# Performance work log

Measured on AMD Instinct MI355X. Metric: run time of the kernel, lower is better.

Reference implementation:

```python
import jax, jax.numpy as jnp
import numpy as np

NEG = -1e9


def setup_inputs() -> dict:
    key = jax.random.key(0)
    kq, kk, kv, ke = jax.random.split(key, 4)
    B, H, S, D = 4, 16, 2048, 64
    q = jax.random.normal(kq, (B, H, S, D), dtype=jnp.float32)
    k = jax.random.normal(kk, (B, H, S, D), dtype=jnp.float32)
    v = jax.random.normal(kv, (B, H, S, D), dtype=jnp.float32)
    event_length = jax.random.randint(ke, (B,), 0, S, dtype=jnp.int32)
    return {"q": q, "k": k, "v": v, "event_length": event_length}


def reference(q, k, v, event_length):
    B, H, S, D = q.shape
    scale = jnp.sqrt(jnp.asarray(D, dtype=jnp.float32))
    # [b,h,s,q] scores
    scores = jnp.einsum('bhsd,bhqd->bhsq', q, k) / scale
    idx = jnp.arange(S)
    el = event_length[:, None]  # [B,1]
    valid = idx[None, :] < el   # [B,S]
    # mask[b,s,q] = valid[b,s] & valid[b,q]; broadcast over heads
    mask = (valid[:, None, :, None] & valid[:, None, None, :])  # [B,1,S,S]
    scores = jnp.where(mask, scores, NEG)
    attn = jax.nn.softmax(scores, axis=-1)
    # dropout p=0.0 (eval): identity
    out = jnp.einsum('bhsq,bhqd->bhsd', attn, v)
    return out
```

## Files before the change

kernel.cpp:

```cpp
#include <hip/hip_runtime.h>
#include <hip/hip_bf16.h>


#define SQ 2048
#define DH 64
#define NBH 64
#define TK 64
#define LDE 72

typedef __attribute__((ext_vector_type(4))) float f32x4;
typedef __attribute__((ext_vector_type(8))) short bf16x8;
typedef __attribute__((ext_vector_type(4))) unsigned int u32x4;
typedef __attribute__((ext_vector_type(2))) unsigned int u32x2;

__device__ __forceinline__ unsigned int pk2(float lo, float hi) {
    __hip_bfloat162 h = __float22bfloat162_rn(float2{lo, hi});
    union { __hip_bfloat162 h; unsigned int u; } c; c.h = h;
    return c.u;
}

__global__ __launch_bounds__(256)
void meanv_k(const float* __restrict__ V, float* __restrict__ MV) {
    const int bh  = blockIdx.x >> 4;
    const int seg = blockIdx.x & 15;
    const float* vp = V + ((size_t)bh * SQ + (size_t)seg * 128) * DH;
    const int c = threadIdx.x & 15;
    const int r = threadIdx.x >> 4;
    const float* p = vp + (size_t)r * DH + c * 4;
    f32x4 s0 = *(const f32x4*)(p);
    f32x4 s1 = *(const f32x4*)(p + 16 * DH);
    f32x4 s2 = *(const f32x4*)(p + 32 * DH);
    f32x4 s3 = *(const f32x4*)(p + 48 * DH);
    s0 += *(const f32x4*)(p + 64 * DH);
    s1 += *(const f32x4*)(p + 80 * DH);
    s2 += *(const f32x4*)(p + 96 * DH);
    s3 += *(const f32x4*)(p + 112 * DH);
    f32x4 s = (s0 + s1) + (s2 + s3);
    __shared__ f32x4 red[16][16];
    red[r][c] = s;
    __syncthreads();
    if (threadIdx.x < 16) {
        f32x4 a = red[0][threadIdx.x];
        #pragma unroll
        for (int j = 1; j < 16; ++j) a += red[j][threadIdx.x];
        const float inv = 1.0f / (float)SQ;
        atomicAdd(&MV[bh * DH + threadIdx.x * 4 + 0], a[0] * inv);
        atomicAdd(&MV[bh * DH + threadIdx.x * 4 + 1], a[1] * inv);
        atomicAdd(&MV[bh * DH + threadIdx.x * 4 + 2], a[2] * inv);
        atomicAdd(&MV[bh * DH + threadIdx.x * 4 + 3], a[3] * inv);
    }
}

__global__ __launch_bounds__(256, 3)
void flash5(const float* __restrict__ Q, const float* __restrict__ K,
            const float* __restrict__ V, const int* __restrict__ EL,
            const float* __restrict__ MV, float* __restrict__ O,
            int* __restrict__ ticket) {
    const int t = threadIdx.x;

    {
        const int bh0    = blockIdx.x & (NBH - 1);
        const int qbase0 = (blockIdx.x >> 6) * 128;
        const int el0    = EL[bh0 >> 4];
        if (qbase0 >= el0) {
            float* Op = O + (size_t)bh0 * SQ * DH;
            const int c16 = t & 15, r0 = t >> 4;
            f32x4 mv = *(const f32x4*)(MV + bh0 * DH + c16 * 4);
            #pragma unroll
            for (int i = 0; i < 8; ++i)
                *(f32x4*)(Op + (size_t)(qbase0 + r0 + i * 16) * DH + c16 * 4) = mv;
        }
    }

    const int el0 = EL[0], el1 = EL[1], el2 = EL[2], el3 = EL[3];
    const int v0 = (el0 + 127) >> 7, v1 = (el1 + 127) >> 7;
    const int v2 = (el2 + 127) >> 7, v3 = (el3 + 127) >> 7;
    const int n0 = 16 * v0, n1 = n0 + 16 * v1, n2 = n1 + 16 * v2;
    const int nvalid = n2 + 16 * v3;

    __shared__ short Kb[TK][LDE];
    __shared__ short Vt[DH][LDE];
    __shared__ short Pl[4][32][LDE];
    __shared__ int item_s;

    const int wq = t >> 6, lane = t & 63, qd = lane >> 4, c = lane & 15;

    const int ksrow = t >> 2;
    const int ksdc  = t & 3;
    const int vpair = t & 31;
    const int vdg   = t >> 5;

    for (;;) {
        if (t == 0) item_s = atomicAdd(ticket, 1);
        __syncthreads();
        const int it = item_s;
        if (it >= nvalid) break;

        int b, u, vb, el;
        if      (it < n0) { b = 0; u = it;      vb = v0; el = el0; }
        else if (it < n1) { b = 1; u = it - n0; vb = v1; el = el1; }
        else if (it < n2) { b = 2; u = it - n1; vb = v2; el = el2; }
        else              { b = 3; u = it - n2; vb = v3; el = el3; }
        const int head  = u / vb;
        const int qt    = u - head * vb;
        const int bh    = b * 16 + head;
        const int qbase = qt * 128;

        const size_t base = (size_t)bh * SQ * DH;
        const float* Qp = Q + base;
        const float* Kp = K + base;
        const float* Vp = V + base;
        float* Op = O + base;

        const float sc = 0.125f * 1.44269504f;
        bf16x8 qf[2][2];
        #pragma unroll
        for (int nt = 0; nt < 2; ++nt) {
            const int row = qbase + wq * 32 + nt * 16 + c;
            #pragma unroll
            for (int kc = 0; kc < 2; ++kc) {
                const float* p = Qp + (size_t)row * DH + kc * 32 + qd * 8;
                f32x4 a  = *(const f32x4*)p;
                f32x4 bb = *(const f32x4*)(p + 4);
                u32x4 f;
                f[0] = pk2(a[0] * sc, a[1] * sc);
                f[1] = pk2(a[2] * sc, a[3] * sc);
                f[2] = pk2(bb[0] * sc, bb[1] * sc);
                f[3] = pk2(bb[2] * sc, bb[3] * sc);
                qf[nt][kc] = *(bf16x8*)&f;
            }
        }

        float l_[2] = {0.f, 0.f};
        f32x4 oacc[4][2];
        #pragma unroll
        for (int dt = 0; dt < 4; ++dt)
            #pragma unroll
            for (int nt = 0; nt < 2; ++nt)
                oacc[dt][nt] = (f32x4){0.f, 0.f, 0.f, 0.f};

        const int nkt = (el + TK - 1) / TK;

        f32x4 kg0, kg1, kg2, kg3, vg0, vg1, vg2, vg3;
        {
            const float* kp = Kp + (size_t)ksrow * DH + ksdc * 16;
            kg0 = *(const f32x4*)kp;
            kg1 = *(const f32x4*)(kp + 4);
            kg2 = *(const f32x4*)(kp + 8);
            kg3 = *(const f32x4*)(kp + 12);
            const float* vp0 = Vp + (size_t)(2 * vpair) * DH + vdg * 8;
            vg0 = *(const f32x4*)vp0;
            vg1 = *(const f32x4*)(vp0 + 4);
            vg2 = *(const f32x4*)(vp0 + DH);
            vg3 = *(const f32x4*)(vp0 + DH + 4);
        }

        for (int kt = 0; kt < nkt; ++kt) {
            const int k0 = kt * TK;

            __syncthreads();
            {
                u32x4 w0, w1;
                w0[0] = pk2(kg0[0], kg0[1]); w0[1] = pk2(kg0[2], kg0[3]);
                w0[2] = pk2(kg1[0], kg1[1]); w0[3] = pk2(kg1[2], kg1[3]);
                w1[0] = pk2(kg2[0], kg2[1]); w1[1] = pk2(kg2[2], kg2[3]);
                w1[2] = pk2(kg3[0], kg3[1]); w1[3] = pk2(kg3[2], kg3[3]);
                *(u32x4*)&Kb[ksrow][ksdc * 16]     = w0;
                *(u32x4*)&Kb[ksrow][ksdc * 16 + 8] = w1;
            }
            {
                #pragma unroll
                for (int i = 0; i < 4; ++i) {
                    *(unsigned int*)&Vt[vdg * 8 + i][2 * vpair]     = pk2(vg0[i], vg2[i]);
                    *(unsigned int*)&Vt[vdg * 8 + 4 + i][2 * vpair] = pk2(vg1[i], vg3[i]);
                }
            }
            __syncthreads();

            if (kt + 1 < nkt) {
                const int kn = k0 + TK;
                const float* kp = Kp + (size_t)(kn + ksrow) * DH + ksdc * 16;
                kg0 = *(const f32x4*)kp;
                kg1 = *(const f32x4*)(kp + 4);
                kg2 = *(const f32x4*)(kp + 8);
                kg3 = *(const f32x4*)(kp + 12);
                const float* vp0 = Vp + (size_t)(kn + 2 * vpair) * DH + vdg * 8;
                vg0 = *(const f32x4*)vp0;
                vg1 = *(const f32x4*)(vp0 + 4);
                vg2 = *(const f32x4*)(vp0 + DH);
                vg3 = *(const f32x4*)(vp0 + DH + 4);
            }

            f32x4 st[4][2];
            #pragma unroll
            for (int mt = 0; mt < 4; ++mt) {
                bf16x8 a0 = *(const bf16x8*)&Kb[mt * 16 + c][qd * 8];
                bf16x8 a1 = *(const bf16x8*)&Kb[mt * 16 + c][32 + qd * 8];
                #pragma unroll
                for (int nt = 0; nt < 2; ++nt) {
                    f32x4 acc = (f32x4){0.f, 0.f, 0.f, 0.f};
                    acc = __builtin_amdgcn_mfma_f32_16x16x32_bf16(a0, qf[nt][0], acc, 0, 0, 0);
                    acc = __builtin_amdgcn_mfma_f32_16x16x32_bf16(a1, qf[nt][1], acc, 0, 0, 0);
                    st[mt][nt] = acc;
                }
            }

            if (k0 + TK > el) {
                #pragma unroll
                for (int mt = 0; mt < 4; ++mt)
                    #pragma unroll
                    for (int r = 0; r < 4; ++r)
                        if (k0 + mt * 16 + qd * 4 + r >= el) {
                            st[mt][0][r] = -1e30f;
                            st[mt][1][r] = -1e30f;
                        }
            }

            #pragma unroll
            for (int nt = 0; nt < 2; ++nt) {
                #pragma unroll
                for (int mt = 0; mt < 4; ++mt) {
                    const float p0 = exp2f(st[mt][nt][0]);
                    const float p1 = exp2f(st[mt][nt][1]);
                    const float p2 = exp2f(st[mt][nt][2]);
                    const float p3 = exp2f(st[mt][nt][3]);
                    l_[nt] += (p0 + p1) + (p2 + p3);
                    u32x2 pw;
                    pw[0] = pk2(p0, p1);
                    pw[1] = pk2(p2, p3);
                    *(u32x2*)&Pl[wq][nt * 16 + c][mt * 16 + qd * 4] = pw;
                }
            }

            #pragma unroll
            for (int kc = 0; kc < 2; ++kc) {
                bf16x8 pb0 = *(const bf16x8*)&Pl[wq][c][kc * 32 + qd * 8];
                bf16x8 pb1 = *(const bf16x8*)&Pl[wq][16 + c][kc * 32 + qd * 8];
                #pragma unroll
                for (int dt = 0; dt < 4; ++dt) {
                    bf16x8 vf = *(const bf16x8*)&Vt[dt * 16 + c][kc * 32 + qd * 8];
                    oacc[dt][0] = __builtin_amdgcn_mfma_f32_16x16x32_bf16(vf, pb0, oacc[dt][0], 0, 0, 0);
                    oacc[dt][1] = __builtin_amdgcn_mfma_f32_16x16x32_bf16(vf, pb1, oacc[dt][1], 0, 0, 0);
                }
            }
        }

        #pragma unroll
        for (int nt = 0; nt < 2; ++nt) {
            l_[nt] += __shfl_xor(l_[nt], 16);
            l_[nt] += __shfl_xor(l_[nt], 32);
        }

        #pragma unroll
        for (int nt = 0; nt < 2; ++nt) {
            const int row = qbase + wq * 32 + nt * 16 + c;
            if (row < el) {
                const float inv = 1.0f / l_[nt];
                #pragma unroll
                for (int dt = 0; dt < 4; ++dt) {
                    f32x4 o = oacc[dt][nt];
                    o[0] *= inv; o[1] *= inv; o[2] *= inv; o[3] *= inv;
                    *(f32x4*)(Op + (size_t)row * DH + dt * 16 + qd * 4) = o;
                }
            } else {
                #pragma unroll
                for (int dt = 0; dt < 4; ++dt) {
                    f32x4 mv = *(const f32x4*)(MV + bh * DH + dt * 16 + qd * 4);
                    *(f32x4*)(Op + (size_t)row * DH + dt * 16 + qd * 4) = mv;
                }
            }
        }
    }
}

extern "C" void kernel_launch(void* const* d_in, const int* in_sizes, int n_in,
                              void* d_out, int out_size, void* d_ws, size_t ws_size,
                              hipStream_t stream) {
    const float* q  = (const float*)d_in[0];
    const float* k  = (const float*)d_in[1];
    const float* v  = (const float*)d_in[2];
    const int*   el = (const int*)d_in[3];
    float* out = (float*)d_out;
    float* mv  = (float*)d_ws;
    int*   tk  = (int*)((char*)d_ws + NBH * DH * sizeof(float));

    hipMemsetAsync(d_ws, 0, NBH * DH * sizeof(float) + 64, stream);
    meanv_k<<<dim3(NBH * 16), dim3(256), 0, stream>>>(v, mv);
    flash5<<<dim3(NBH * (SQ / 128)), dim3(256), 0, stream>>>(q, k, v, el, mv, out, tk);
}
```

Measured before the change: 203.3 us.

## Pre-convert K/V to swizzled bf16 tiles and stream them with async LDS loads

Adds a prepass kernel that converts K and V to bf16 in a pre-swizzled, pre-transposed tile layout and fuses the mean-of-V computation into it. The main attention kernel then uses 512-thread blocks with 8 waves and double-buffered direct global-to-LDS async copies, so the fp32 conversion and transpose no longer run inside the inner loop. This spends an extra workspace pass and 16 MB of scratch in exchange for halving the K/V bytes read per tile and overlapping loads with MFMA. The old path is kept as a fallback when the workspace is too small.

```diff
diff --git a/kernel.cpp b/kernel.cpp
--- a/kernel.cpp
+++ b/kernel.cpp
@@ -6,7 +6,10 @@
 #define DH 64
 #define NBH 64
 #define TK 64
+#define NTILE 32
+#define TILE_B 8192
 #define LDE 72
+#define LVP 68
 
 typedef __attribute__((ext_vector_type(4))) float f32x4;
 typedef __attribute__((ext_vector_type(8))) short bf16x8;
@@ -18,6 +21,257 @@
     union { __hip_bfloat162 h; unsigned int u; } c; c.h = h;
     return c.u;
 }
+
+__device__ __forceinline__ float bfu16_to_f(unsigned short s) {
+    union { unsigned int u; float f; } c; c.u = ((unsigned int)s) << 16;
+    return c.f;
+}
+
+__device__ __forceinline__ void async_cp16(const void* g, void* l) {
+    __builtin_amdgcn_global_load_lds(
+        (const __attribute__((address_space(1))) unsigned int*)g,
+        (__attribute__((address_space(3))) unsigned int*)l, 16, 0, 0);
+}
+
+
+__global__ __launch_bounds__(256)
+void convkv(const float* __restrict__ K, const float* __restrict__ V,
+            const int* __restrict__ EL, float* __restrict__ MV,
+            char* __restrict__ Kbt, char* __restrict__ Vbt) {
+    const int bh = blockIdx.x >> 5;
+    const int kt = blockIdx.x & 31;
+    const int k0 = kt * TK;
+    const int el = EL[bh >> 4];
+    const int t = threadIdx.x;
+    const int r  = t >> 2;
+    const int dc = t & 3;
+
+    __shared__ short LV[64][LVP];
+
+    {
+        const float* vp = V + ((size_t)bh * SQ + k0 + r) * DH + dc * 16;
+        f32x4 a = *(const f32x4*)vp;
+        f32x4 b = *(const f32x4*)(vp + 4);
+        f32x4 c2 = *(const f32x4*)(vp + 8);
+        f32x4 d2 = *(const f32x4*)(vp + 12);
+        u32x4 w0, w1;
+        w0[0] = pk2(a[0], a[1]);  w0[1] = pk2(a[2], a[3]);
+        w0[2] = pk2(b[0], b[1]);  w0[3] = pk2(b[2], b[3]);
+        w1[0] = pk2(c2[0], c2[1]); w1[1] = pk2(c2[2], c2[3]);
+        w1[2] = pk2(d2[0], d2[1]); w1[3] = pk2(d2[2], d2[3]);
+        *(u32x4*)&LV[r][dc * 16]     = w0;
+        *(u32x4*)&LV[r][dc * 16 + 8] = w1;
+    }
+
+    if (k0 < el) {
+        const float* kp = K + ((size_t)bh * SQ + k0 + r) * DH + dc * 16;
+        f32x4 a = *(const f32x4*)kp;
+        f32x4 b = *(const f32x4*)(kp + 4);
+        f32x4 c2 = *(const f32x4*)(kp + 8);
+        f32x4 d2 = *(const f32x4*)(kp + 12);
+        u32x4 w0, w1;
+        w0[0] = pk2(a[0], a[1]);  w0[1] = pk2(a[2], a[3]);
+        w0[2] = pk2(b[0], b[1]);  w0[3] = pk2(b[2], b[3]);
+        w1[0] = pk2(c2[0], c2[1]); w1[1] = pk2(c2[2], c2[3]);
+        w1[2] = pk2(d2[0], d2[1]); w1[3] = pk2(d2[2], d2[3]);
+        char* kb = Kbt + (size_t)(bh * NTILE + kt) * TILE_B + r * 128;
+        *(u32x4*)(kb + (((dc * 2)     ^ (r & 7)) << 4)) = w0;
+        *(u32x4*)(kb + (((dc * 2 + 1) ^ (r & 7)) << 4)) = w1;
+    }
+
+    __syncthreads();
+
+    const int dd  = t >> 2;
+    const int seg = t & 3;
+    float msum = 0.f;
+    unsigned int wv[8];
+    #pragma unroll
+    for (int i = 0; i < 8; ++i) {
+        const int pos = seg * 16 + 2 * i;
+        const int key = (pos & ~31) | ((pos & 4) << 2) | ((pos & 24) >> 1) | (pos & 3);
+        const unsigned short s0 = (unsigned short)LV[key][dd];
+        const unsigned short s1 = (unsigned short)LV[key + 1][dd];
+        msum += bfu16_to_f(s0) + bfu16_to_f(s1);
+        wv[i] = (unsigned int)s0 | ((unsigned int)s1 << 16);
+    }
+    msum += __shfl_xor(msum, 1);
+    msum += __shfl_xor(msum, 2);
+    if (seg == 0) atomicAdd(&MV[bh * DH + dd], msum * (1.0f / (float)SQ));
+
+    if (k0 < el) {
+        char* vb = Vbt + (size_t)(bh * NTILE + kt) * TILE_B + dd * 128;
+        u32x4 o0 = {wv[0], wv[1], wv[2], wv[3]};
+        u32x4 o1 = {wv[4], wv[5], wv[6], wv[7]};
+        *(u32x4*)(vb + (((seg * 2)     ^ (dd & 7)) << 4)) = o0;
+        *(u32x4*)(vb + (((seg * 2 + 1) ^ (dd & 7)) << 4)) = o1;
+    }
+}
+
+__global__ __launch_bounds__(512, 4)
+void flash6(const float* __restrict__ Q, const int* __restrict__ EL,
+            const float* __restrict__ MV, float* __restrict__ O,
+            const char* __restrict__ Kbt, const char* __restrict__ Vbt,
+            int* __restrict__ ticket) {
+    const int t = threadIdx.x;
+
+    {
+        const int bh0 = blockIdx.x & (NBH - 1);
+        const int qb0 = (blockIdx.x >> 6) * 128;
+        const int elb = EL[bh0 >> 4];
+        if (qb0 >= elb) {
+            float* Op = O + (size_t)bh0 * SQ * DH;
+            const int c16 = t & 15, r0 = t >> 4;
+            f32x4 mv = *(const f32x4*)(MV + bh0 * DH + c16 * 4);
+            #pragma unroll
+            for (int i = 0; i < 4; ++i)
+                *(f32x4*)(Op + (size_t)(qb0 + r0 + i * 32) * DH + c16 * 4) = mv;
+        }
+    }
+
+    const int el0 = EL[0], el1 = EL[1], el2 = EL[2], el3 = EL[3];
+    const int v0 = (el0 + 127) >> 7, v1 = (el1 + 127) >> 7;
+    const int v2 = (el2 + 127) >> 7, v3 = (el3 + 127) >> 7;
+    const int n0 = 16 * v0, n1 = n0 + 16 * v1, n2 = n1 + 16 * v2;
+    const int nvalid = n2 + 16 * v3;
+
+    __shared__ short KT[2][TK * DH];
+    __shared__ short VT[2][TK * DH];
+    __shared__ int item_s;
+
+    const int wq = t >> 6, lane = t & 63, qd = lane >> 4, c = lane & 15;
+    const int cs = c & 7;
+
+    for (;;) {
+        if (t == 0) item_s = atomicAdd(ticket, 1);
+        __syncthreads();
+        const int it = item_s;
+        if (it >= nvalid) break;
+
+        int b, u, vb, el;
+        if      (it < n0) { b = 0; u = it;      vb = v0; el = el0; }
+        else if (it < n1) { b = 1; u = it - n0; vb = v1; el = el1; }
+        else if (it < n2) { b = 2; u = it - n1; vb = v2; el = el2; }
+        else              { b = 3; u = it - n2; vb = v3; el = el3; }
+        const int head  = u / vb;
+        const int qt    = u - head * vb;
+        const int bh    = b * 16 + head;
+        const int qbase = qt * 128;
+
+        const float* Qp = Q + (size_t)bh * SQ * DH;
+        float*       Op = O + (size_t)bh * SQ * DH;
+        const char*  Kt = Kbt + (size_t)bh * NTILE * TILE_B;
+        const char*  Vt = Vbt + (size_t)bh * NTILE * TILE_B;
+
+        const float sc = 0.125f * 1.44269504f;
+        const int qrow = qbase + wq * 16 + c;
+        bf16x8 qf[2];
+        #pragma unroll
+        for (int kc = 0; kc < 2; ++kc) {
+            const float* p = Qp + (size_t)qrow * DH + kc * 32 + qd * 8;
+            f32x4 a  = *(const f32x4*)p;
+            f32x4 bq = *(const f32x4*)(p + 4);
+            u32x4 f;
+            f[0] = pk2(a[0] * sc, a[1] * sc);
+            f[1] = pk2(a[2] * sc, a[3] * sc);
+            f[2] = pk2(bq[0] * sc, bq[1] * sc);
+            f[3] = pk2(bq[2] * sc, bq[3] * sc);
+            qf[kc] = *(bf16x8*)&f;
+        }
+
+        float l_ = 0.f;
+        f32x4 oacc[4];
+        #pragma unroll
+        for (int dt = 0; dt < 4; ++dt) oacc[dt] = (f32x4){0.f, 0.f, 0.f, 0.f};
+
+        const int nkt = (el + TK - 1) >> 6;
+
+        {
+            async_cp16(Kt + (size_t)t * 16, (char*)&KT[0][0] + wq * 1024);
+            async_cp16(Vt + (size_t)t * 16, (char*)&VT[0][0] + wq * 1024);
+        }
+        asm volatile("s_waitcnt vmcnt(0)" ::: "memory");
+        __syncthreads();
+
+        int buf = 0;
+        for (int kt = 0; kt < nkt; ++kt) {
+            if (kt + 1 < nkt) {
+                const char* gK = Kt + (size_t)(kt + 1) * TILE_B + t * 16;
+                const char* gV = Vt + (size_t)(kt + 1) * TILE_B + t * 16;
+                async_cp16(gK, (char*)&KT[buf ^ 1][0] + wq * 1024);
+                async_cp16(gV, (char*)&VT[buf ^ 1][0] + wq * 1024);
+            }
+            const int k0 = kt * TK;
+
+            const char* Kb = (const char*)&KT[buf][0];
+            f32x4 st[4];
+            #pragma unroll
+            for (int mt = 0; mt < 4; ++mt) {
+                const char* rp = Kb + (mt * 16 + c) * 128;
+                bf16x8 a0 = *(const bf16x8*)(rp + (((qd)     ^ cs) << 4));
+                bf16x8 a1 = *(const bf16x8*)(rp + (((qd + 4) ^ cs) << 4));
+                f32x4 acc = (f32x4){0.f, 0.f, 0.f, 0.f};
+                acc = __builtin_amdgcn_mfma_f32_16x16x32_bf16(a0, qf[0], acc, 0, 0, 0);
+                acc = __builtin_amdgcn_mfma_f32_16x16x32_bf16(a1, qf[1], acc, 0, 0, 0);
+                st[mt] = acc;
+            }
+
+            if (k0 + TK > el) {
+                #pragma unroll
+                for (int mt = 0; mt < 4; ++mt)
+                    #pragma unroll
+                    for (int r = 0; r < 4; ++r)
+                        if (k0 + mt * 16 + qd * 4 + r >= el) st[mt][r] = -1e30f;
+            }
+
+            u32x4 pw[2];
+            #pragma unroll
+            for (int mt = 0; mt < 4; ++mt) {
+                const float p0 = exp2f(st[mt][0]);
+                const float p1 = exp2f(st[mt][1]);
+                const float p2 = exp2f(st[mt][2]);
+                const float p3 = exp2f(st[mt][3]);
+                l_ += (p0 + p1) + (p2 + p3);
+                pw[mt >> 1][(mt & 1) * 2]     = pk2(p0, p1);
+                pw[mt >> 1][(mt & 1) * 2 + 1] = pk2(p2, p3);
+            }
+
+            const char* Vb = (const char*)&VT[buf][0];
+            #pragma unroll
+            for (int kc = 0; kc < 2; ++kc) {
+                bf16x8 pb = *(bf16x8*)&pw[kc];
+                #pragma unroll
+                for (int dt = 0; dt < 4; ++dt) {
+                    const char* vp = Vb + (dt * 16 + c) * 128 + (((kc * 4 + qd) ^ cs) << 4);
+                    bf16x8 vf = *(const bf16x8*)vp;
+                    oacc[dt] = __builtin_amdgcn_mfma_f32_16x16x32_bf16(vf, pb, oacc[dt], 0, 0, 0);
+                }
+            }
+
+            asm volatile("s_waitcnt vmcnt(0)" ::: "memory");
+            __syncthreads();
+            buf ^= 1;
+        }
+
+        l_ += __shfl_xor(l_, 16);
+        l_ += __shfl_xor(l_, 32);
+
+        if (qrow < el) {
+            const float inv = 1.0f / l_;
+            #pragma unroll
+            for (int dt = 0; dt < 4; ++dt) {
+                f32x4 o = oacc[dt];
+                o[0] *= inv; o[1] *= inv; o[2] *= inv; o[3] *= inv;
+                *(f32x4*)(Op + (size_t)qrow * DH + dt * 16 + qd * 4) = o;
+            }
+        } else {
+            #pragma unroll
+            for (int dt = 0; dt < 4; ++dt)
+                *(f32x4*)(Op + (size_t)qrow * DH + dt * 16 + qd * 4) =
+                    *(const f32x4*)(MV + bh * DH + dt * 16 + qd * 4);
+        }
+    }
+}
+
 
 __global__ __launch_bounds__(256)
 void meanv_k(const float* __restrict__ V, float* __restrict__ MV) {
@@ -57,12 +311,11 @@
             const float* __restrict__ MV, float* __restrict__ O,
             int* __restrict__ ticket) {
     const int t = threadIdx.x;
-
     {
         const int bh0    = blockIdx.x & (NBH - 1);
         const int qbase0 = (blockIdx.x >> 6) * 128;
-        const int el0    = EL[bh0 >> 4];
-        if (qbase0 >= el0) {
+        const int elb    = EL[bh0 >> 4];
+        if (qbase0 >= elb) {
             float* Op = O + (size_t)bh0 * SQ * DH;
             const int c16 = t & 15, r0 = t >> 4;
             f32x4 mv = *(const f32x4*)(MV + bh0 * DH + c16 * 4);
@@ -84,7 +337,6 @@
     __shared__ int item_s;
 
     const int wq = t >> 6, lane = t & 63, qd = lane >> 4, c = lane & 15;
-
     const int ksrow = t >> 2;
     const int ksdc  = t & 3;
     const int vpair = t & 31;
@@ -273,6 +525,7 @@
     }
 }
 
+
 extern "C" void kernel_launch(void* const* d_in, const int* in_sizes, int n_in,
                               void* d_out, int out_size, void* d_ws, size_t ws_size,
                               hipStream_t stream) {
@@ -281,10 +534,25 @@
     const float* v  = (const float*)d_in[2];
     const int*   el = (const int*)d_in[3];
     float* out = (float*)d_out;
-    float* mv  = (float*)d_ws;
-    int*   tk  = (int*)((char*)d_ws + NBH * DH * sizeof(float));
-
-    hipMemsetAsync(d_ws, 0, NBH * DH * sizeof(float) + 64, stream);
-    meanv_k<<<dim3(NBH * 16), dim3(256), 0, stream>>>(v, mv);
-    flash5<<<dim3(NBH * (SQ / 128)), dim3(256), 0, stream>>>(q, k, v, el, mv, out, tk);
-}
+
+    const size_t kbt_bytes = (size_t)NBH * NTILE * TILE_B;
+    const size_t needed    = 65536 + 2 * kbt_bytes;
+
+    if (ws_size >= needed) {
+        float* mv  = (float*)d_ws;
+        int*   tk  = (int*)((char*)d_ws + 16384);
+        char*  kbt = (char*)d_ws + 65536;
+        char*  vbt = kbt + kbt_bytes;
+
+        hipMemsetAsync(d_ws, 0, 65536, stream);
+        convkv<<<dim3(NBH * NTILE), dim3(256), 0, stream>>>(k, v, el, mv, kbt, vbt);
+        flash6<<<dim3(NBH * (SQ / 128)), dim3(512), 0, stream>>>(q, el, mv, out, kbt, vbt, tk);
+    } else {
+        float* mv = (float*)d_ws;
+        int*   tk = (int*)((char*)d_ws + NBH * DH * sizeof(float));
+
+        hipMemsetAsync(d_ws, 0, NBH * DH * sizeof(float) + 64, stream);
+        meanv_k<<<dim3(NBH * 16), dim3(256), 0, stream>>>(v, mv);
+        flash5<<<dim3(NBH * (SQ / 128)), dim3(256), 0, stream>>>(q, k, v, el, mv, out, tk);
+    }
+}
```

After: 194.2 us. 1.05x faster.
